# Kernel tuning notes

Hardware: AMD Instinct MI355X
Metric: run time of the kernel (lower is better)

## Reference

```python
import jax, jax.numpy as jnp
import numpy as np

D = 1024      # n_embd
NH = 16       # attention heads
E = 8         # n_experts
K = 2         # k_best
FF = 4 * D    # expert MLP hidden
EPS = 1e-6    # rms_norm_epsilon
TEMP = 1.0    # target_temperature


def setup_inputs() -> dict:
    key = jax.random.key(0)
    ks = jax.random.split(key, 12)
    B, S = 2, 1024
    s = 0.02
    return {
        "x": jax.random.normal(ks[0], (B, S, D), jnp.float32),
        "attn_norm_w": jnp.ones((D,), jnp.float32),
        "wq": jax.random.normal(ks[1], (D, D), jnp.float32) * s,
        "wk": jax.random.normal(ks[2], (D, D), jnp.float32) * s,
        "wv": jax.random.normal(ks[3], (D, D), jnp.float32) * s,
        "wo": jax.random.normal(ks[4], (D, D), jnp.float32) * s,
        "mlp_norm_w": jnp.ones((D,), jnp.float32),
        "router_w": jax.random.normal(ks[5], (D, E), jnp.float32) * s,
        "w1": jax.random.normal(ks[6], (E, D, FF), jnp.float32) * s,
        "b1": jnp.zeros((E, FF), jnp.float32),
        "w2": jax.random.normal(ks[7], (E, FF, D), jnp.float32) * s,
        "b2": jnp.zeros((E, D), jnp.float32),
    }


def _rmsnorm(x, w):
    var = jnp.mean(jnp.square(x), axis=-1, keepdims=True)
    return x * jax.lax.rsqrt(var + EPS) * w


def _attention(x, wq, wk, wv, wo):
    B, S, _ = x.shape
    dh = D // NH
    q = (x @ wq).reshape(B, S, NH, dh)
    k = (x @ wk).reshape(B, S, NH, dh)
    v = (x @ wv).reshape(B, S, NH, dh)
    scores = jnp.einsum("bqhd,bkhd->bhqk", q, k) / jnp.sqrt(jnp.float32(dh))
    causal = jnp.tril(jnp.ones((S, S), bool))  # [S,S]
    scores = jnp.where(causal[None, None], scores, jnp.finfo(scores.dtype).min)
    attn = jax.nn.softmax(scores, axis=-1)
    out = jnp.einsum("bhqk,bkhd->bqhd", attn, v).reshape(B, S, D)
    return out @ wo


def reference(x, attn_norm_w, wq, wk, wv, wo, mlp_norm_w, router_w, w1, b1, w2, b2):
    B, S, _ = x.shape
    # attention sub-block
    x = x + _attention(_rmsnorm(x, attn_norm_w), wq, wk, wv, wo)
    residual = x
    h = _rmsnorm(x, mlp_norm_w)  # [B,S,D]

    # router: temperature softmax + top-k
    logits = h @ router_w / TEMP                      # [B,S,E]
    probs = jax.nn.softmax(logits, axis=-1)
    top_k_scores, top_k_indices = jax.lax.top_k(probs, K)  # [B,S,K]
    onehot = jax.nn.one_hot(top_k_indices, E, dtype=h.dtype)  # [B,S,K,E]
    gates = jnp.einsum("bsk,bske->bse", top_k_scores, onehot)  # [B,S,E]

    # load-balancing loss (Switch-style) + expert counts
    counts = jnp.sum(onehot, axis=(0, 1, 2))          # [E]
    frac = counts / (B * S * K)
    mean_prob = jnp.mean(probs, axis=(0, 1))          # [E]
    balancing_loss = E * jnp.sum(frac * mean_prob)

    # experts: dense dispatch; tokens with zero gate contribute nothing,
    # so this matches the sort/gather/scatter top-k combine exactly.
    pre = jnp.einsum("bsd,edf->ebsf", h, w1) + b1[:, None, None]  # [E,B,S,FF]
    act = jax.nn.gelu(pre)
    y = jnp.einsum("ebsf,efd->ebsd", act, w2) + b2[:, None, None]  # [E,B,S,D]
    moe = jnp.einsum("ebsd,bse->bsd", y, gates)

    out = residual + moe
    return out, balancing_loss, counts
```

## Files before the change

### kernel.cpp

```cpp
#include <hip/hip_runtime.h>

typedef __bf16 bf16;
typedef __bf16 bf16x8 __attribute__((ext_vector_type(8)));
typedef float f32x4 __attribute__((ext_vector_type(4)));

#define D_   1024
#define S_   1024
#define B_   2
#define NTOK 2048
#define FF_  4096
#define NE   8
#define CAP  5120
#define OUTN 2097152

__device__ __forceinline__ float gelu_f(float x) {
    return 0.5f * x * (1.0f + tanhf(0.7978845608028654f * (x + 0.044715f * x * x * x)));
}

__global__ __launch_bounds__(256) void rmsnorm_k(const float* __restrict__ x,
                                                 const float* __restrict__ w,
                                                 float* __restrict__ yf,
                                                 bf16* __restrict__ yhi,
                                                 bf16* __restrict__ ylo) {
    int row = blockIdx.x;
    int t = threadIdx.x;
    const float* xr = x + (size_t)row * D_;
    float4 v = *(const float4*)(xr + t * 4);
    float ss = v.x * v.x + v.y * v.y + v.z * v.z + v.w * v.w;
    for (int off = 32; off; off >>= 1) ss += __shfl_down(ss, off);
    __shared__ float wsum[4];
    if ((t & 63) == 0) wsum[t >> 6] = ss;
    __syncthreads();
    float tot = wsum[0] + wsum[1] + wsum[2] + wsum[3];
    float rr = rsqrtf(tot * (1.0f / D_) + 1e-6f);
    float4 wv = *(const float4*)(w + t * 4);
    float y[4];
    y[0] = v.x * rr * wv.x; y[1] = v.y * rr * wv.y;
    y[2] = v.z * rr * wv.z; y[3] = v.w * rr * wv.w;
    if (yf) *(float4*)(yf + (size_t)row * D_ + t * 4) = *(float4*)y;
    if (yhi) {
#pragma unroll
        for (int i = 0; i < 4; i++) {
            bf16 hi = (bf16)y[i];
            yhi[(size_t)row * D_ + t * 4 + i] = hi;
            if (ylo) ylo[(size_t)row * D_ + t * 4 + i] = (bf16)(y[i] - (float)hi);
        }
    }
}

__global__ __launch_bounds__(256) void trans_split_k(
    const float* __restrict__ w0, const float* __restrict__ w1p,
    const float* __restrict__ w2p, const float* __restrict__ w3,
    bf16* o0h, bf16* o0l, bf16* o1h, bf16* o1l,
    bf16* o2h, bf16* o2l, bf16* o3h, bf16* o3l) {
    int z = blockIdx.z;
    const float* src = (z == 0) ? w0 : (z == 1) ? w1p : (z == 2) ? w2p : w3;
    bf16* dh = (z == 0) ? o0h : (z == 1) ? o1h : (z == 2) ? o2h : o3h;
    bf16* dl = (z == 0) ? o0l : (z == 1) ? o1l : (z == 2) ? o2l : o3l;
    __shared__ float tl[32][33];
    int c0 = blockIdx.x * 32, r0 = blockIdx.y * 32;
    int tx = threadIdx.x & 31, ty = threadIdx.x >> 5;
#pragma unroll
    for (int i = 0; i < 4; i++) {
        int r = ty + i * 8;
        tl[r][tx] = src[(size_t)(r0 + r) * 1024 + c0 + tx];
    }
    __syncthreads();
#pragma unroll
    for (int i = 0; i < 4; i++) {
        int c = ty + i * 8;
        float v = tl[tx][c];
        bf16 hi = (bf16)v;
        dh[(size_t)(c0 + c) * 1024 + r0 + tx] = hi;
        dl[(size_t)(c0 + c) * 1024 + r0 + tx] = (bf16)(v - (float)hi);
    }
}

__global__ __launch_bounds__(256) void transpose_cast_k(const float* __restrict__ in,
                                                        bf16* __restrict__ out,
                                                        int R, int C) {
    __shared__ float tl[32][33];
    size_t base = (size_t)blockIdx.z * R * C;
    const float* src = in + base;
    bf16* dst = out + base;
    int c0 = blockIdx.x * 32, r0 = blockIdx.y * 32;
    int tx = threadIdx.x & 31, tyy = threadIdx.x >> 5;
#pragma unroll
    for (int i = 0; i < 4; i++) {
        int r = tyy + i * 8;
        tl[r][tx] = src[(size_t)(r0 + r) * C + c0 + tx];
    }
    __syncthreads();
#pragma unroll
    for (int i = 0; i < 4; i++) {
        int c = tyy + i * 8;
        dst[(size_t)(c0 + c) * R + r0 + tx] = (bf16)tl[tx][c];
    }
}

#define GLD 40

#define GEMM_SPLIT_BODY(EPILOGUE)                                                     \
    __shared__ bf16 Ash[128 * GLD], Asl[128 * GLD], Bsh[128 * GLD], Bsl[128 * GLD];   \
    int t = threadIdx.x;                                                              \
    int m0 = blockIdx.x * 128, n0 = blockIdx.y * 128;                                 \
    int wv = t >> 6, ln = t & 63, wm = wv >> 1, wn = wv & 1;                          \
    int l15 = ln & 15, qd = ln >> 4;                                                  \
    f32x4 acc[4][4];                                                                  \
    _Pragma("unroll") for (int mt = 0; mt < 4; mt++)                                  \
        _Pragma("unroll") for (int nt = 0; nt < 4; nt++)                              \
            acc[mt][nt] = (f32x4){0.f, 0.f, 0.f, 0.f};                                \
    for (int k0 = 0; k0 < 1024; k0 += 32) {                                           \
        __syncthreads();                                                              \
        _Pragma("unroll") for (int j = 0; j < 2; j++) {                               \
            int idx = t + j * 256;                                                    \
            int row = idx >> 2, kc = (idx & 3) * 8;                                   \
            *(uint4*)&Ash[row * GLD + kc] = *(const uint4*)(Ah + (size_t)(m0 + row) * 1024 + k0 + kc); \
            *(uint4*)&Asl[row * GLD + kc] = *(const uint4*)(Al + (size_t)(m0 + row) * 1024 + k0 + kc); \
            *(uint4*)&Bsh[row * GLD + kc] = *(const uint4*)(Bh + (size_t)(n0 + row) * 1024 + k0 + kc); \
            *(uint4*)&Bsl[row * GLD + kc] = *(const uint4*)(Bl + (size_t)(n0 + row) * 1024 + k0 + kc); \
        }                                                                             \
        __syncthreads();                                                              \
        bf16x8 ah[4], al[4], bh[4], bl[4];                                            \
        _Pragma("unroll") for (int mt = 0; mt < 4; mt++) {                            \
            ah[mt] = *(const bf16x8*)&Ash[(wm * 64 + mt * 16 + l15) * GLD + qd * 8];  \
            al[mt] = *(const bf16x8*)&Asl[(wm * 64 + mt * 16 + l15) * GLD + qd * 8];  \
        }                                                                             \
        _Pragma("unroll") for (int nt = 0; nt < 4; nt++) {                            \
            bh[nt] = *(const bf16x8*)&Bsh[(wn * 64 + nt * 16 + l15) * GLD + qd * 8];  \
            bl[nt] = *(const bf16x8*)&Bsl[(wn * 64 + nt * 16 + l15) * GLD + qd * 8];  \
        }                                                                             \
        _Pragma("unroll") for (int mt = 0; mt < 4; mt++)                              \
            _Pragma("unroll") for (int nt = 0; nt < 4; nt++) {                        \
                acc[mt][nt] = __builtin_amdgcn_mfma_f32_16x16x32_bf16(ah[mt], bh[nt], acc[mt][nt], 0, 0, 0); \
                acc[mt][nt] = __builtin_amdgcn_mfma_f32_16x16x32_bf16(ah[mt], bl[nt], acc[mt][nt], 0, 0, 0); \
                acc[mt][nt] = __builtin_amdgcn_mfma_f32_16x16x32_bf16(al[mt], bh[nt], acc[mt][nt], 0, 0, 0); \
            }                                                                         \
    }                                                                                 \
    _Pragma("unroll") for (int mt = 0; mt < 4; mt++)                                  \
        _Pragma("unroll") for (int nt = 0; nt < 4; nt++) {                            \
            int gn = n0 + wn * 64 + nt * 16 + l15;                                    \
            _Pragma("unroll") for (int r = 0; r < 4; r++) {                           \
                int gm = m0 + wm * 64 + mt * 16 + qd * 4 + r;                         \
                float vv = acc[mt][nt][r];                                            \
                EPILOGUE                                                              \
            }                                                                         \
        }

__global__ __launch_bounds__(256) void gemm_split_qkv_k(
    const bf16* __restrict__ Ah, const bf16* __restrict__ Al,
    const bf16* __restrict__ Bqh, const bf16* __restrict__ Bql,
    const bf16* __restrict__ Bkh, const bf16* __restrict__ Bkl,
    const bf16* __restrict__ Bvh, const bf16* __restrict__ Bvl,
    bf16* Cqh, bf16* Cql, bf16* Ckh, bf16* Ckl, bf16* Cvh, bf16* Cvl) {
    int z = blockIdx.z;
    const bf16* Bh = (z == 0) ? Bqh : (z == 1) ? Bkh : Bvh;
    const bf16* Bl = (z == 0) ? Bql : (z == 1) ? Bkl : Bvl;
    bf16* Ch = (z == 0) ? Cqh : (z == 1) ? Ckh : Cvh;
    bf16* Cl = (z == 0) ? Cql : (z == 1) ? Ckl : Cvl;
    GEMM_SPLIT_BODY({
        bf16 hi = (bf16)vv;
        Ch[(size_t)gm * D_ + gn] = hi;
        Cl[(size_t)gm * D_ + gn] = (bf16)(vv - (float)hi);
    })
}

__global__ __launch_bounds__(256) void gemm_split_wo_k(
    const bf16* __restrict__ Ah, const bf16* __restrict__ Al,
    const bf16* __restrict__ Bh, const bf16* __restrict__ Bl,
    float* __restrict__ C, const float* __restrict__ X) {
    GEMM_SPLIT_BODY({
        C[(size_t)gm * D_ + gn] = X[(size_t)gm * D_ + gn] + vv;
    })
}

#define AP 72

__global__ __launch_bounds__(256) void attn_mfma_k(
    const bf16* __restrict__ qhp, const bf16* __restrict__ qlp,
    const bf16* __restrict__ khp, const bf16* __restrict__ klp,
    const bf16* __restrict__ vhp, const bf16* __restrict__ vlp,
    bf16* __restrict__ aoh, bf16* __restrict__ aol) {
    int qt = blockIdx.x, h = blockIdx.y, b = blockIdx.z;
    __shared__ bf16 Ksh[64 * AP], Ksl[64 * AP], VTh[64 * AP], VTl[64 * AP];
    __shared__ bf16 Ph[4][16 * AP], Pl[4][16 * AP];
    int t = threadIdx.x, wv = t >> 6, ln = t & 63, l15 = ln & 15, qd = ln >> 4;

    bf16x8 aqh[2], aql[2];
    {
        size_t qb = ((size_t)(b * S_ + qt * 64 + wv * 16 + l15)) * D_ + h * 64 + qd * 8;
        aqh[0] = *(const bf16x8*)(qhp + qb);
        aqh[1] = *(const bf16x8*)(qhp + qb + 32);
        aql[0] = *(const bf16x8*)(qlp + qb);
        aql[1] = *(const bf16x8*)(qlp + qb + 32);
    }
    f32x4 oacc[4];
    float mrow[4], lrow[4];
#pragma unroll
    for (int i = 0; i < 4; i++) {
        oacc[i] = (f32x4){0.f, 0.f, 0.f, 0.f};
        mrow[i] = -1e30f; lrow[i] = 0.0f;
    }

    for (int kt = 0; kt <= qt; kt++) {
        __syncthreads();
#pragma unroll
        for (int j = 0; j < 2; j++) {
            int idx = t + j * 256;
            int row = idx >> 3, ch = (idx & 7) * 8;
            size_t g = ((size_t)(b * S_ + kt * 64 + row)) * D_ + h * 64 + ch;
            *(uint4*)&Ksh[row * AP + ch] = *(const uint4*)(khp + g);
            *(uint4*)&Ksl[row * AP + ch] = *(const uint4*)(klp + g);
            bf16x8 vvh = *(const bf16x8*)(vhp + g);
            bf16x8 vvl = *(const bf16x8*)(vlp + g);
#pragma unroll
            for (int jj = 0; jj < 8; jj++) {
                VTh[(ch + jj) * AP + row] = vvh[jj];
                VTl[(ch + jj) * AP + row] = vvl[jj];
            }
        }
        __syncthreads();

        f32x4 sacc[4];
#pragma unroll
        for (int nt = 0; nt < 4; nt++) sacc[nt] = (f32x4){0.f, 0.f, 0.f, 0.f};
#pragma unroll
        for (int ks = 0; ks < 2; ks++) {
#pragma unroll
            for (int nt = 0; nt < 4; nt++) {
                bf16x8 bh = *(const bf16x8*)&Ksh[(nt * 16 + l15) * AP + ks * 32 + qd * 8];
                bf16x8 bl = *(const bf16x8*)&Ksl[(nt * 16 + l15) * AP + ks * 32 + qd * 8];
                sacc[nt] = __builtin_amdgcn_mfma_f32_16x16x32_bf16(aqh[ks], bh, sacc[nt], 0, 0, 0);
                sacc[nt] = __builtin_amdgcn_mfma_f32_16x16x32_bf16(aqh[ks], bl, sacc[nt], 0, 0, 0);
                sacc[nt] = __builtin_amdgcn_mfma_f32_16x16x32_bf16(aql[ks], bh, sacc[nt], 0, 0, 0);
            }
        }
        bool diag = (kt == qt);
#pragma unroll
        for (int r = 0; r < 4; r++) {
            float s0[4];
#pragma unroll
            for (int nt = 0; nt < 4; nt++) {
                s0[nt] = sacc[nt][r] * 0.125f;
                if (diag && (nt * 16 + l15) > (wv * 16 + qd * 4 + r)) s0[nt] = -1e30f;
            }
            float vmax = fmaxf(fmaxf(s0[0], s0[1]), fmaxf(s0[2], s0[3]));
            for (int off = 1; off < 16; off <<= 1) vmax = fmaxf(vmax, __shfl_xor(vmax, off));
            float mnew = fmaxf(mrow[r], vmax);
            float alpha = expf(mrow[r] - mnew);
            float p[4], rs = 0.0f;
#pragma unroll
            for (int nt = 0; nt < 4; nt++) { p[nt] = expf(s0[nt] - mnew); rs += p[nt]; }
            for (int off = 1; off < 16; off <<= 1) rs += __shfl_xor(rs, off);
            lrow[r] = lrow[r] * alpha + rs;
            mrow[r] = mnew;
#pragma unroll
            for (int nt = 0; nt < 4; nt++) oacc[nt][r] *= alpha;
            int prow = qd * 4 + r;
#pragma unroll
            for (int nt = 0; nt < 4; nt++) {
                bf16 hi = (bf16)p[nt];
                Ph[wv][prow * AP + nt * 16 + l15] = hi;
                Pl[wv][prow * AP + nt * 16 + l15] = (bf16)(p[nt] - (float)hi);
            }
        }
#pragma unroll
        for (int ks2 = 0; ks2 < 2; ks2++) {
            bf16x8 aph = *(const bf16x8*)&Ph[wv][l15 * AP + ks2 * 32 + qd * 8];
            bf16x8 apl = *(const bf16x8*)&Pl[wv][l15 * AP + ks2 * 32 + qd * 8];
#pragma unroll
            for (int nt = 0; nt < 4; nt++) {
                bf16x8 bvh = *(const bf16x8*)&VTh[(nt * 16 + l15) * AP + ks2 * 32 + qd * 8];
                bf16x8 bvl = *(const bf16x8*)&VTl[(nt * 16 + l15) * AP + ks2 * 32 + qd * 8];
                oacc[nt] = __builtin_amdgcn_mfma_f32_16x16x32_bf16(aph, bvh, oacc[nt], 0, 0, 0);
                oacc[nt] = __builtin_amdgcn_mfma_f32_16x16x32_bf16(aph, bvl, oacc[nt], 0, 0, 0);
                oacc[nt] = __builtin_amdgcn_mfma_f32_16x16x32_bf16(apl, bvh, oacc[nt], 0, 0, 0);
            }
        }
    }

#pragma unroll
    for (int r = 0; r < 4; r++) {
        float inv = 1.0f / lrow[r];
        size_t rowa = ((size_t)(b * S_ + qt * 64 + wv * 16 + qd * 4 + r)) * D_ + h * 64;
#pragma unroll
        for (int nt = 0; nt < 4; nt++) {
            float o = oacc[nt][r] * inv;
            bf16 hi = (bf16)o;
            aoh[rowa + nt * 16 + l15] = hi;
            aol[rowa + nt * 16 + l15] = (bf16)(o - (float)hi);
        }
    }
}

__global__ __launch_bounds__(256) void router_k(const float* __restrict__ h,
                                                const float* __restrict__ rw,
                                                int* __restrict__ tidx,
                                                float* __restrict__ tgate,
                                                int* __restrict__ ecnt,
                                                float* __restrict__ psum) {
    int wv = threadIdx.x >> 6, ln = threadIdx.x & 63;
    int tok = blockIdx.x * 4 + wv;
    const float* hr = h + (size_t)tok * D_;
    float acc[NE];
#pragma unroll
    for (int e = 0; e < NE; e++) acc[e] = 0.0f;
    int base = ln * 16;
#pragma unroll
    for (int c = 0; c < 4; c++) {
        float4 hv = *(const float4*)(hr + base + c * 4);
        const float* rp = rw + (size_t)(base + c * 4) * NE;
        float hx[4] = {hv.x, hv.y, hv.z, hv.w};
#pragma unroll
        for (int jj = 0; jj < 4; jj++)
#pragma unroll
            for (int e = 0; e < NE; e++)
                acc[e] = fmaf(hx[jj], rp[jj * NE + e], acc[e]);
    }
#pragma unroll
    for (int e = 0; e < NE; e++)
        for (int off = 32; off; off >>= 1) acc[e] += __shfl_down(acc[e], off);

    __shared__ float pb[4][NE];
    if (ln == 0) {
        float mx = acc[0];
#pragma unroll
        for (int e = 1; e < NE; e++) mx = fmaxf(mx, acc[e]);
        float p[NE], ssum = 0.0f;
#pragma unroll
        for (int e = 0; e < NE; e++) { p[e] = expf(acc[e] - mx); ssum += p[e]; }
        float inv = 1.0f / ssum;
#pragma unroll
        for (int e = 0; e < NE; e++) p[e] *= inv;
        int i0 = 0; float b0 = p[0];
#pragma unroll
        for (int e = 1; e < NE; e++) if (p[e] > b0) { b0 = p[e]; i0 = e; }
        int i1 = -1; float b1v = -1.0f;
#pragma unroll
        for (int e = 0; e < NE; e++) if (e != i0 && p[e] > b1v) { b1v = p[e]; i1 = e; }
        tidx[tok * 2] = i0; tidx[tok * 2 + 1] = i1;
        tgate[tok * 2] = b0; tgate[tok * 2 + 1] = b1v;
        atomicAdd(&ecnt[i0], 1);
        atomicAdd(&ecnt[i1], 1);
#pragma unroll
        for (int e = 0; e < NE; e++) pb[wv][e] = p[e];
    }
    __syncthreads();
    if (threadIdx.x < NE) {
        float s2 = pb[0][threadIdx.x] + pb[1][threadIdx.x] + pb[2][threadIdx.x] + pb[3][threadIdx.x];
        atomicAdd(&psum[threadIdx.x], s2);
    }
}

__global__ void passb_k(const int* __restrict__ ecnt, const float* __restrict__ psum,
                        int* __restrict__ eoffp, int* __restrict__ ecnt2,
                        float* __restrict__ out_tail) {
    if (threadIdx.x == 0) {
        int off = 0; float loss = 0.0f;
        for (int e = 0; e < NE; e++) {
            eoffp[e] = off;
            int c = ecnt[e];
            off += (c + 127) & ~127;
            loss += (c * (1.0f / 4096.0f)) * (psum[e] * (1.0f / 2048.0f));
            out_tail[1 + e] = (float)c;
            ecnt2[e] = 0;
        }
        eoffp[NE] = off;
        out_tail[0] = 8.0f * loss;
    }
}

__global__ __launch_bounds__(256) void scatter_k(const int* __restrict__ tidx,
                                                 const float* __restrict__ tgate,
                                                 const int* __restrict__ eoffp,
                                                 int* __restrict__ ecnt2,
                                                 int* __restrict__ stok,
                                                 float* __restrict__ sgate) {
    int tok = blockIdx.x * 256 + threadIdx.x;
    for (int k = 0; k < 2; k++) {
        int e = tidx[tok * 2 + k];
        int pos = eoffp[e] + atomicAdd(&ecnt2[e], 1);
        stok[pos] = tok;
        sgate[pos] = tgate[tok * 2 + k];
    }
}

#define MLD 40

__global__ __launch_bounds__(256) void moe_gemm1_k(const bf16* __restrict__ hB,
                                                   const bf16* __restrict__ w1t,
                                                   const float* __restrict__ b1,
                                                   const int* __restrict__ eoffp,
                                                   const int* __restrict__ stok,
                                                   bf16* __restrict__ act) {
    int m0 = blockIdx.x * 128, n0 = blockIdx.y * 128;
    if (m0 >= eoffp[NE]) return;
    int e = 0;
#pragma unroll
    for (int i = 1; i < NE; i++) if (m0 >= eoffp[i]) e = i;

    __shared__ bf16 As[128 * MLD];
    __shared__ bf16 Bs[128 * MLD];
    __shared__ int tok_l[128];
    int t = threadIdx.x;
    if (t < 128) tok_l[t] = stok[m0 + t];

    int wv = t >> 6, ln = t & 63;
    int wm = wv >> 1, wn = wv & 1;
    int lane15 = ln & 15, quad = ln >> 4;
    f32x4 acc[4][4];
#pragma unroll
    for (int mt = 0; mt < 4; mt++)
#pragma unroll
        for (int nt = 0; nt < 4; nt++) acc[mt][nt] = (f32x4){0.f, 0.f, 0.f, 0.f};

    const bf16* Bbase = w1t + ((size_t)e * FF_ + n0) * D_;

    for (int k0 = 0; k0 < D_; k0 += 32) {
        __syncthreads();
#pragma unroll
        for (int j = 0; j < 2; j++) {
            int idx = t + j * 256;
            int row = idx >> 2, kc = (idx & 3) * 8;
            uint4 av = *(const uint4*)(hB + (size_t)tok_l[row] * D_ + k0 + kc);
            *(uint4*)&As[row * MLD + kc] = av;
            uint4 bv = *(const uint4*)(Bbase + (size_t)row * D_ + k0 + kc);
            *(uint4*)&Bs[row * MLD + kc] = bv;
        }
        __syncthreads();
        bf16x8 af[4], bfr[4];
#pragma unroll
        for (int mt = 0; mt < 4; mt++)
            af[mt] = *(const bf16x8*)&As[(wm * 64 + mt * 16 + lane15) * MLD + quad * 8];
#pragma unroll
        for (int nt = 0; nt < 4; nt++)
            bfr[nt] = *(const bf16x8*)&Bs[(wn * 64 + nt * 16 + lane15) * MLD + quad * 8];
#pragma unroll
        for (int mt = 0; mt < 4; mt++)
#pragma unroll
            for (int nt = 0; nt < 4; nt++)
                acc[mt][nt] = __builtin_amdgcn_mfma_f32_16x16x32_bf16(af[mt], bfr[nt], acc[mt][nt], 0, 0, 0);
    }

    const float* b1e = b1 + (size_t)e * FF_;
#pragma unroll
    for (int mt = 0; mt < 4; mt++)
#pragma unroll
        for (int nt = 0; nt < 4; nt++) {
            int gn = n0 + wn * 64 + nt * 16 + lane15;
            float bias = b1e[gn];
#pragma unroll
            for (int r = 0; r < 4; r++) {
                int gm = m0 + wm * 64 + mt * 16 + quad * 4 + r;
                float vv = acc[mt][nt][r] + bias;
                act[(size_t)gm * FF_ + gn] = (bf16)gelu_f(vv);
            }
        }
}

__global__ __launch_bounds__(256) void moe_gemm2_k(const bf16* __restrict__ act,
                                                   const bf16* __restrict__ w2t,
                                                   const float* __restrict__ b2,
                                                   const int* __restrict__ eoffp,
                                                   const int* __restrict__ stok,
                                                   const float* __restrict__ sgate,
                                                   float* __restrict__ out) {
    int m0 = blockIdx.x * 128, n0 = blockIdx.y * 128;
    if (m0 >= eoffp[NE]) return;
    int e = 0;
#pragma unroll
    for (int i = 1; i < NE; i++) if (m0 >= eoffp[i]) e = i;

    __shared__ bf16 As[128 * MLD];
    __shared__ bf16 Bs[128 * MLD];
    __shared__ int tok_l[128];
    __shared__ float gate_l[128];
    int t = threadIdx.x;
    if (t < 128) { tok_l[t] = stok[m0 + t]; gate_l[t] = sgate[m0 + t]; }

    int wv = t >> 6, ln = t & 63;
    int wm = wv >> 1, wn = wv & 1;
    int lane15 = ln & 15, quad = ln >> 4;
    f32x4 acc[4][4];
#pragma unroll
    for (int mt = 0; mt < 4; mt++)
#pragma unroll
        for (int nt = 0; nt < 4; nt++) acc[mt][nt] = (f32x4){0.f, 0.f, 0.f, 0.f};

    const bf16* Bbase = w2t + ((size_t)e * D_ + n0) * FF_;

    for (int k0 = 0; k0 < FF_; k0 += 32) {
        __syncthreads();
#pragma unroll
        for (int j = 0; j < 2; j++) {
            int idx = t + j * 256;
            int row = idx >> 2, kc = (idx & 3) * 8;
            uint4 av = *(const uint4*)(act + (size_t)(m0 + row) * FF_ + k0 + kc);
            *(uint4*)&As[row * MLD + kc] = av;
            uint4 bv = *(const uint4*)(Bbase + (size_t)row * FF_ + k0 + kc);
            *(uint4*)&Bs[row * MLD + kc] = bv;
        }
        __syncthreads();
        bf16x8 af[4], bfr[4];
#pragma unroll
        for (int mt = 0; mt < 4; mt++)
            af[mt] = *(const bf16x8*)&As[(wm * 64 + mt * 16 + lane15) * MLD + quad * 8];
#pragma unroll
        for (int nt = 0; nt < 4; nt++)
            bfr[nt] = *(const bf16x8*)&Bs[(wn * 64 + nt * 16 + lane15) * MLD + quad * 8];
#pragma unroll
        for (int mt = 0; mt < 4; mt++)
#pragma unroll
            for (int nt = 0; nt < 4; nt++)
                acc[mt][nt] = __builtin_amdgcn_mfma_f32_16x16x32_bf16(af[mt], bfr[nt], acc[mt][nt], 0, 0, 0);
    }

    const float* b2e = b2 + (size_t)e * D_;
#pragma unroll
    for (int mt = 0; mt < 4; mt++)
#pragma unroll
        for (int nt = 0; nt < 4; nt++) {
            int gn = n0 + wn * 64 + nt * 16 + lane15;
            float bias = b2e[gn];
#pragma unroll
            for (int r = 0; r < 4; r++) {
                int lm = wm * 64 + mt * 16 + quad * 4 + r;
                int tok = tok_l[lm];
                float g = gate_l[lm];
                atomicAdd(out + (size_t)tok * D_ + gn, g * (acc[mt][nt][r] + bias));
            }
        }
}

extern "C" void kernel_launch(void* const* d_in, const int* in_sizes, int n_in,
                              void* d_out, int out_size, void* d_ws, size_t ws_size,
                              hipStream_t stream) {
    const float* x   = (const float*)d_in[0];
    const float* anw = (const float*)d_in[1];
    const float* wq  = (const float*)d_in[2];
    const float* wk  = (const float*)d_in[3];
    const float* wv  = (const float*)d_in[4];
    const float* wo  = (const float*)d_in[5];
    const float* mnw = (const float*)d_in[6];
    const float* rw  = (const float*)d_in[7];
    const float* w1  = (const float*)d_in[8];
    const float* b1  = (const float*)d_in[9];
    const float* w2  = (const float*)d_in[10];
    const float* b2  = (const float*)d_in[11];
    float* out = (float*)d_out;

    char* p = (char*)d_ws;
    auto take = [&](size_t n) { char* r = p; p += (n + 255) & ~(size_t)255; return r; };
    bf16* h1h = (bf16*)take((size_t)OUTN * 2);
    bf16* h1l = (bf16*)take((size_t)OUTN * 2);
    bf16* qh  = (bf16*)take((size_t)OUTN * 2);
    bf16* ql  = (bf16*)take((size_t)OUTN * 2);
    bf16* kh  = (bf16*)take((size_t)OUTN * 2);
    bf16* kl  = (bf16*)take((size_t)OUTN * 2);
    bf16* vh  = (bf16*)take((size_t)OUTN * 2);
    bf16* vl  = (bf16*)take((size_t)OUTN * 2);
    bf16* wqth = (bf16*)take((size_t)D_ * D_ * 2);
    bf16* wqtl = (bf16*)take((size_t)D_ * D_ * 2);
    bf16* wkth = (bf16*)take((size_t)D_ * D_ * 2);
    bf16* wktl = (bf16*)take((size_t)D_ * D_ * 2);
    bf16* wvth = (bf16*)take((size_t)D_ * D_ * 2);
    bf16* wvtl = (bf16*)take((size_t)D_ * D_ * 2);
    bf16* woth = (bf16*)take((size_t)D_ * D_ * 2);
    bf16* wotl = (bf16*)take((size_t)D_ * D_ * 2);
    bf16* w1t = (bf16*)take((size_t)NE * FF_ * D_ * 2);
    bf16* w2t = (bf16*)take((size_t)NE * FF_ * D_ * 2);
    bf16* act = (bf16*)take((size_t)CAP * FF_ * 2);
    int*   tidx  = (int*)take(NTOK * 2 * 4);
    float* tgate = (float*)take(NTOK * 2 * 4);
    int*   ecnt  = (int*)take(64);
    int*   ecnt2 = (int*)take(64);
    float* psum  = (float*)take(64);
    int*   eoffp = (int*)take(64);
    int*   stok  = (int*)take(CAP * 4);
    float* sgate = (float*)take(CAP * 4);

    bf16*  aoh = h1h;
    bf16*  aol = h1l;
    float* h_f = (float*)qh;
    bf16*  h_b = kh;

    hipMemsetAsync(ecnt, 0, NE * 4, stream);
    hipMemsetAsync(psum, 0, NE * 4, stream);
    hipMemsetAsync(stok, 0, CAP * 4, stream);
    hipMemsetAsync(sgate, 0, CAP * 4, stream);

    trans_split_k<<<dim3(32, 32, 4), 256, 0, stream>>>(wq, wk, wv, wo,
        wqth, wqtl, wkth, wktl, wvth, wvtl, woth, wotl);
    transpose_cast_k<<<dim3(FF_ / 32, D_ / 32, NE), 256, 0, stream>>>(w1, w1t, D_, FF_);
    transpose_cast_k<<<dim3(D_ / 32, FF_ / 32, NE), 256, 0, stream>>>(w2, w2t, FF_, D_);

    rmsnorm_k<<<NTOK, 256, 0, stream>>>(x, anw, nullptr, h1h, h1l);
    gemm_split_qkv_k<<<dim3(16, 8, 3), 256, 0, stream>>>(h1h, h1l,
        wqth, wqtl, wkth, wktl, wvth, wvtl,
        qh, ql, kh, kl, vh, vl);
    attn_mfma_k<<<dim3(16, 16, 2), 256, 0, stream>>>(qh, ql, kh, kl, vh, vl, aoh, aol);
    gemm_split_wo_k<<<dim3(16, 8), 256, 0, stream>>>(aoh, aol, woth, wotl, out, x);

    rmsnorm_k<<<NTOK, 256, 0, stream>>>(out, mnw, h_f, h_b, nullptr);
    router_k<<<NTOK / 4, 256, 0, stream>>>(h_f, rw, tidx, tgate, ecnt, psum);
    passb_k<<<1, 64, 0, stream>>>(ecnt, psum, eoffp, ecnt2, out + OUTN);
    scatter_k<<<NTOK / 256, 256, 0, stream>>>(tidx, tgate, eoffp, ecnt2, stok, sgate);
    moe_gemm1_k<<<dim3(CAP / 128, FF_ / 128), 256, 0, stream>>>(h_b, w1t, b1, eoffp, stok, act);
    moe_gemm2_k<<<dim3(CAP / 128, D_ / 128), 256, 0, stream>>>(act, w2t, b2, eoffp, stok, sgate, out);
}
```

Before: 900.1 us.

## Shrink GEMM tiles to 64x64, reverse attention tile order, replace atomic MoE combine

Switches the QKV, Wo and MoE second GEMMs from 128x128 to 64x64 tiles, giving four times as many workgroups on a device with many CUs. The attention grid now runs the heaviest causal query tiles first so the tail is better balanced. The MoE down-projection writes per-slot outputs to a buffer, and a separate combine kernel gathers each token's two expert rows with their gates, replacing scattered float atomics and making the result deterministic. In exchange, smaller tiles mean less operand reuse per block, and the combine adds an extra pass over the slot buffer.

```diff
diff --git a/kernel.cpp b/kernel.cpp
--- a/kernel.cpp
+++ b/kernel.cpp
@@ -100,77 +100,67 @@
 
 #define GLD 40
 
-#define GEMM_SPLIT_BODY(EPILOGUE)                                                     \
-    __shared__ bf16 Ash[128 * GLD], Asl[128 * GLD], Bsh[128 * GLD], Bsl[128 * GLD];   \
-    int t = threadIdx.x;                                                              \
-    int m0 = blockIdx.x * 128, n0 = blockIdx.y * 128;                                 \
-    int wv = t >> 6, ln = t & 63, wm = wv >> 1, wn = wv & 1;                          \
-    int l15 = ln & 15, qd = ln >> 4;                                                  \
-    f32x4 acc[4][4];                                                                  \
-    _Pragma("unroll") for (int mt = 0; mt < 4; mt++)                                  \
-        _Pragma("unroll") for (int nt = 0; nt < 4; nt++)                              \
-            acc[mt][nt] = (f32x4){0.f, 0.f, 0.f, 0.f};                                \
-    for (int k0 = 0; k0 < 1024; k0 += 32) {                                           \
-        __syncthreads();                                                              \
-        _Pragma("unroll") for (int j = 0; j < 2; j++) {                               \
-            int idx = t + j * 256;                                                    \
-            int row = idx >> 2, kc = (idx & 3) * 8;                                   \
-            *(uint4*)&Ash[row * GLD + kc] = *(const uint4*)(Ah + (size_t)(m0 + row) * 1024 + k0 + kc); \
-            *(uint4*)&Asl[row * GLD + kc] = *(const uint4*)(Al + (size_t)(m0 + row) * 1024 + k0 + kc); \
-            *(uint4*)&Bsh[row * GLD + kc] = *(const uint4*)(Bh + (size_t)(n0 + row) * 1024 + k0 + kc); \
-            *(uint4*)&Bsl[row * GLD + kc] = *(const uint4*)(Bl + (size_t)(n0 + row) * 1024 + k0 + kc); \
-        }                                                                             \
-        __syncthreads();                                                              \
-        bf16x8 ah[4], al[4], bh[4], bl[4];                                            \
-        _Pragma("unroll") for (int mt = 0; mt < 4; mt++) {                            \
-            ah[mt] = *(const bf16x8*)&Ash[(wm * 64 + mt * 16 + l15) * GLD + qd * 8];  \
-            al[mt] = *(const bf16x8*)&Asl[(wm * 64 + mt * 16 + l15) * GLD + qd * 8];  \
-        }                                                                             \
-        _Pragma("unroll") for (int nt = 0; nt < 4; nt++) {                            \
-            bh[nt] = *(const bf16x8*)&Bsh[(wn * 64 + nt * 16 + l15) * GLD + qd * 8];  \
-            bl[nt] = *(const bf16x8*)&Bsl[(wn * 64 + nt * 16 + l15) * GLD + qd * 8];  \
-        }                                                                             \
-        _Pragma("unroll") for (int mt = 0; mt < 4; mt++)                              \
-            _Pragma("unroll") for (int nt = 0; nt < 4; nt++) {                        \
-                acc[mt][nt] = __builtin_amdgcn_mfma_f32_16x16x32_bf16(ah[mt], bh[nt], acc[mt][nt], 0, 0, 0); \
-                acc[mt][nt] = __builtin_amdgcn_mfma_f32_16x16x32_bf16(ah[mt], bl[nt], acc[mt][nt], 0, 0, 0); \
-                acc[mt][nt] = __builtin_amdgcn_mfma_f32_16x16x32_bf16(al[mt], bh[nt], acc[mt][nt], 0, 0, 0); \
-            }                                                                         \
-    }                                                                                 \
-    _Pragma("unroll") for (int mt = 0; mt < 4; mt++)                                  \
-        _Pragma("unroll") for (int nt = 0; nt < 4; nt++) {                            \
-            int gn = n0 + wn * 64 + nt * 16 + l15;                                    \
-            _Pragma("unroll") for (int r = 0; r < 4; r++) {                           \
-                int gm = m0 + wm * 64 + mt * 16 + qd * 4 + r;                         \
-                float vv = acc[mt][nt][r];                                            \
-                EPILOGUE                                                              \
-            }                                                                         \
-        }
-
-__global__ __launch_bounds__(256) void gemm_split_qkv_k(
+#define GEMM64_SPLIT_BODY(N0EXPR, EPILOGUE)                                            \
+    __shared__ bf16 Ash[64 * GLD], Asl[64 * GLD], Bsh[64 * GLD], Bsl[64 * GLD];        \
+    int t = threadIdx.x;                                                               \
+    int m0 = blockIdx.x * 64;                                                          \
+    int n0 = (N0EXPR);                                                                 \
+    int wv = t >> 6, ln = t & 63, l15 = ln & 15, qd = ln >> 4;                         \
+    int srow = t >> 2, skc = (t & 3) * 8;                                              \
+    f32x4 acc[4];                                                                      \
+    _Pragma("unroll") for (int mt = 0; mt < 4; mt++) acc[mt] = (f32x4){0.f,0.f,0.f,0.f}; \
+    for (int k0 = 0; k0 < 1024; k0 += 32) {                                            \
+        __syncthreads();                                                               \
+        *(bf16x8*)&Ash[srow * GLD + skc] = *(const bf16x8*)(Ah + (size_t)(m0 + srow) * 1024 + k0 + skc); \
+        *(bf16x8*)&Asl[srow * GLD + skc] = *(const bf16x8*)(Al + (size_t)(m0 + srow) * 1024 + k0 + skc); \
+        *(bf16x8*)&Bsh[srow * GLD + skc] = *(const bf16x8*)(Bh + (size_t)(n0 + srow) * 1024 + k0 + skc); \
+        *(bf16x8*)&Bsl[srow * GLD + skc] = *(const bf16x8*)(Bl + (size_t)(n0 + srow) * 1024 + k0 + skc); \
+        __syncthreads();                                                               \
+        bf16x8 ah[4], al[4];                                                           \
+        _Pragma("unroll") for (int mt = 0; mt < 4; mt++) {                             \
+            ah[mt] = *(const bf16x8*)&Ash[(mt * 16 + l15) * GLD + qd * 8];             \
+            al[mt] = *(const bf16x8*)&Asl[(mt * 16 + l15) * GLD + qd * 8];             \
+        }                                                                              \
+        bf16x8 bh = *(const bf16x8*)&Bsh[(wv * 16 + l15) * GLD + qd * 8];              \
+        bf16x8 bl = *(const bf16x8*)&Bsl[(wv * 16 + l15) * GLD + qd * 8];              \
+        _Pragma("unroll") for (int mt = 0; mt < 4; mt++) {                             \
+            acc[mt] = __builtin_amdgcn_mfma_f32_16x16x32_bf16(ah[mt], bh, acc[mt], 0, 0, 0); \
+            acc[mt] = __builtin_amdgcn_mfma_f32_16x16x32_bf16(ah[mt], bl, acc[mt], 0, 0, 0); \
+            acc[mt] = __builtin_amdgcn_mfma_f32_16x16x32_bf16(al[mt], bh, acc[mt], 0, 0, 0); \
+        }                                                                              \
+    }                                                                                  \
+    int gnl = wv * 16 + l15;                                                           \
+    _Pragma("unroll") for (int mt = 0; mt < 4; mt++)                                   \
+        _Pragma("unroll") for (int r = 0; r < 4; r++) {                                \
+            int gm = m0 + mt * 16 + qd * 4 + r;                                        \
+            float vv = acc[mt][r];                                                     \
+            EPILOGUE                                                                   \
+        }
+
+__global__ __launch_bounds__(256) void gemm_qkv_k(
     const bf16* __restrict__ Ah, const bf16* __restrict__ Al,
     const bf16* __restrict__ Bqh, const bf16* __restrict__ Bql,
     const bf16* __restrict__ Bkh, const bf16* __restrict__ Bkl,
     const bf16* __restrict__ Bvh, const bf16* __restrict__ Bvl,
     bf16* Cqh, bf16* Cql, bf16* Ckh, bf16* Ckl, bf16* Cvh, bf16* Cvl) {
-    int z = blockIdx.z;
-    const bf16* Bh = (z == 0) ? Bqh : (z == 1) ? Bkh : Bvh;
-    const bf16* Bl = (z == 0) ? Bql : (z == 1) ? Bkl : Bvl;
-    bf16* Ch = (z == 0) ? Cqh : (z == 1) ? Ckh : Cvh;
-    bf16* Cl = (z == 0) ? Cql : (z == 1) ? Ckl : Cvl;
-    GEMM_SPLIT_BODY({
+    int gy = blockIdx.y, zw = gy >> 4;
+    const bf16* Bh = (zw == 0) ? Bqh : (zw == 1) ? Bkh : Bvh;
+    const bf16* Bl = (zw == 0) ? Bql : (zw == 1) ? Bkl : Bvl;
+    bf16* Ch = (zw == 0) ? Cqh : (zw == 1) ? Ckh : Cvh;
+    bf16* Cl = (zw == 0) ? Cql : (zw == 1) ? Ckl : Cvl;
+    GEMM64_SPLIT_BODY((gy & 15) * 64, {
         bf16 hi = (bf16)vv;
-        Ch[(size_t)gm * D_ + gn] = hi;
-        Cl[(size_t)gm * D_ + gn] = (bf16)(vv - (float)hi);
+        Ch[(size_t)gm * D_ + n0 + gnl] = hi;
+        Cl[(size_t)gm * D_ + n0 + gnl] = (bf16)(vv - (float)hi);
     })
 }
 
-__global__ __launch_bounds__(256) void gemm_split_wo_k(
+__global__ __launch_bounds__(256) void gemm_wo_k(
     const bf16* __restrict__ Ah, const bf16* __restrict__ Al,
     const bf16* __restrict__ Bh, const bf16* __restrict__ Bl,
     float* __restrict__ C, const float* __restrict__ X) {
-    GEMM_SPLIT_BODY({
-        C[(size_t)gm * D_ + gn] = X[(size_t)gm * D_ + gn] + vv;
+    GEMM64_SPLIT_BODY(blockIdx.y * 64, {
+        C[(size_t)gm * D_ + n0 + gnl] = X[(size_t)gm * D_ + n0 + gnl] + vv;
     })
 }
 
@@ -181,7 +171,8 @@
     const bf16* __restrict__ khp, const bf16* __restrict__ klp,
     const bf16* __restrict__ vhp, const bf16* __restrict__ vlp,
     bf16* __restrict__ aoh, bf16* __restrict__ aol) {
-    int qt = blockIdx.x, h = blockIdx.y, b = blockIdx.z;
+    int qt = (int)gridDim.x - 1 - (int)blockIdx.x;
+    int h = blockIdx.y, b = blockIdx.z;
     __shared__ bf16 Ksh[64 * AP], Ksl[64 * AP], VTh[64 * AP], VTl[64 * AP];
     __shared__ bf16 Ph[4][16 * AP], Pl[4][16 * AP];
     int t = threadIdx.x, wv = t >> 6, ln = t & 63, l15 = ln & 15, qd = ln >> 4;
@@ -209,8 +200,8 @@
             int idx = t + j * 256;
             int row = idx >> 3, ch = (idx & 7) * 8;
             size_t g = ((size_t)(b * S_ + kt * 64 + row)) * D_ + h * 64 + ch;
-            *(uint4*)&Ksh[row * AP + ch] = *(const uint4*)(khp + g);
-            *(uint4*)&Ksl[row * AP + ch] = *(const uint4*)(klp + g);
+            *(bf16x8*)&Ksh[row * AP + ch] = *(const bf16x8*)(khp + g);
+            *(bf16x8*)&Ksl[row * AP + ch] = *(const bf16x8*)(klp + g);
             bf16x8 vvh = *(const bf16x8*)(vhp + g);
             bf16x8 vvl = *(const bf16x8*)(vlp + g);
 #pragma unroll
@@ -371,17 +362,16 @@
 }
 
 __global__ __launch_bounds__(256) void scatter_k(const int* __restrict__ tidx,
-                                                 const float* __restrict__ tgate,
                                                  const int* __restrict__ eoffp,
                                                  int* __restrict__ ecnt2,
                                                  int* __restrict__ stok,
-                                                 float* __restrict__ sgate) {
+                                                 int* __restrict__ sidx) {
     int tok = blockIdx.x * 256 + threadIdx.x;
     for (int k = 0; k < 2; k++) {
         int e = tidx[tok * 2 + k];
         int pos = eoffp[e] + atomicAdd(&ecnt2[e], 1);
         stok[pos] = tok;
-        sgate[pos] = tgate[tok * 2 + k];
+        sidx[tok * 2 + k] = pos;
     }
 }
 
@@ -462,74 +452,68 @@
                                                    const bf16* __restrict__ w2t,
                                                    const float* __restrict__ b2,
                                                    const int* __restrict__ eoffp,
-                                                   const int* __restrict__ stok,
-                                                   const float* __restrict__ sgate,
-                                                   float* __restrict__ out) {
-    int m0 = blockIdx.x * 128, n0 = blockIdx.y * 128;
+                                                   float* __restrict__ y) {
+    int m0 = blockIdx.x * 64;
     if (m0 >= eoffp[NE]) return;
     int e = 0;
 #pragma unroll
     for (int i = 1; i < NE; i++) if (m0 >= eoffp[i]) e = i;
-
-    __shared__ bf16 As[128 * MLD];
-    __shared__ bf16 Bs[128 * MLD];
-    __shared__ int tok_l[128];
-    __shared__ float gate_l[128];
+    int n0 = blockIdx.y * 64;
+
+    __shared__ bf16 As[64 * MLD];
+    __shared__ bf16 Bs[64 * MLD];
     int t = threadIdx.x;
-    if (t < 128) { tok_l[t] = stok[m0 + t]; gate_l[t] = sgate[m0 + t]; }
-
-    int wv = t >> 6, ln = t & 63;
-    int wm = wv >> 1, wn = wv & 1;
-    int lane15 = ln & 15, quad = ln >> 4;
-    f32x4 acc[4][4];
-#pragma unroll
-    for (int mt = 0; mt < 4; mt++)
-#pragma unroll
-        for (int nt = 0; nt < 4; nt++) acc[mt][nt] = (f32x4){0.f, 0.f, 0.f, 0.f};
+    int wv = t >> 6, ln = t & 63, l15 = ln & 15, qd = ln >> 4;
+    int srow = t >> 2, skc = (t & 3) * 8;
+
+    f32x4 acc[4];
+#pragma unroll
+    for (int mt = 0; mt < 4; mt++) acc[mt] = (f32x4){0.f, 0.f, 0.f, 0.f};
 
     const bf16* Bbase = w2t + ((size_t)e * D_ + n0) * FF_;
 
     for (int k0 = 0; k0 < FF_; k0 += 32) {
         __syncthreads();
-#pragma unroll
-        for (int j = 0; j < 2; j++) {
-            int idx = t + j * 256;
-            int row = idx >> 2, kc = (idx & 3) * 8;
-            uint4 av = *(const uint4*)(act + (size_t)(m0 + row) * FF_ + k0 + kc);
-            *(uint4*)&As[row * MLD + kc] = av;
-            uint4 bv = *(const uint4*)(Bbase + (size_t)row * FF_ + k0 + kc);
-            *(uint4*)&Bs[row * MLD + kc] = bv;
-        }
+        *(bf16x8*)&As[srow * MLD + skc] = *(const bf16x8*)(act + (size_t)(m0 + srow) * FF_ + k0 + skc);
+        *(bf16x8*)&Bs[srow * MLD + skc] = *(const bf16x8*)(Bbase + (size_t)srow * FF_ + k0 + skc);
         __syncthreads();
-        bf16x8 af[4], bfr[4];
+        bf16x8 af[4];
 #pragma unroll
         for (int mt = 0; mt < 4; mt++)
-            af[mt] = *(const bf16x8*)&As[(wm * 64 + mt * 16 + lane15) * MLD + quad * 8];
-#pragma unroll
-        for (int nt = 0; nt < 4; nt++)
-            bfr[nt] = *(const bf16x8*)&Bs[(wn * 64 + nt * 16 + lane15) * MLD + quad * 8];
+            af[mt] = *(const bf16x8*)&As[(mt * 16 + l15) * MLD + qd * 8];
+        bf16x8 bfr = *(const bf16x8*)&Bs[(wv * 16 + l15) * MLD + qd * 8];
 #pragma unroll
         for (int mt = 0; mt < 4; mt++)
-#pragma unroll
-            for (int nt = 0; nt < 4; nt++)
-                acc[mt][nt] = __builtin_amdgcn_mfma_f32_16x16x32_bf16(af[mt], bfr[nt], acc[mt][nt], 0, 0, 0);
-    }
-
-    const float* b2e = b2 + (size_t)e * D_;
+            acc[mt] = __builtin_amdgcn_mfma_f32_16x16x32_bf16(af[mt], bfr, acc[mt], 0, 0, 0);
+    }
+
+    int gn = n0 + wv * 16 + l15;
+    float bias = b2[(size_t)e * D_ + gn];
 #pragma unroll
     for (int mt = 0; mt < 4; mt++)
 #pragma unroll
-        for (int nt = 0; nt < 4; nt++) {
-            int gn = n0 + wn * 64 + nt * 16 + lane15;
-            float bias = b2e[gn];
-#pragma unroll
-            for (int r = 0; r < 4; r++) {
-                int lm = wm * 64 + mt * 16 + quad * 4 + r;
-                int tok = tok_l[lm];
-                float g = gate_l[lm];
-                atomicAdd(out + (size_t)tok * D_ + gn, g * (acc[mt][nt][r] + bias));
-            }
-        }
+        for (int r = 0; r < 4; r++) {
+            int gm = m0 + mt * 16 + qd * 4 + r;
+            y[(size_t)gm * D_ + gn] = acc[mt][r] + bias;
+        }
+}
+
+__global__ __launch_bounds__(256) void combine_k(const float* __restrict__ y,
+                                                 const int* __restrict__ sidx,
+                                                 const float* __restrict__ tgate,
+                                                 float* __restrict__ out) {
+    int tok = blockIdx.x;
+    int d = threadIdx.x * 4;
+    int s0 = sidx[tok * 2], s1 = sidx[tok * 2 + 1];
+    float g0 = tgate[tok * 2], g1 = tgate[tok * 2 + 1];
+    float4 a = *(const float4*)(y + (size_t)s0 * D_ + d);
+    float4 b = *(const float4*)(y + (size_t)s1 * D_ + d);
+    float4 o = *(const float4*)(out + (size_t)tok * D_ + d);
+    o.x += g0 * a.x + g1 * b.x;
+    o.y += g0 * a.y + g1 * b.y;
+    o.z += g0 * a.z + g1 * b.z;
+    o.w += g0 * a.w + g1 * b.w;
+    *(float4*)(out + (size_t)tok * D_ + d) = o;
 }
 
 extern "C" void kernel_launch(void* const* d_in, const int* in_sizes, int n_in,
@@ -572,22 +556,22 @@
     bf16* act = (bf16*)take((size_t)CAP * FF_ * 2);
     int*   tidx  = (int*)take(NTOK * 2 * 4);
     float* tgate = (float*)take(NTOK * 2 * 4);
+    int*   sidx  = (int*)take(NTOK * 2 * 4);
     int*   ecnt  = (int*)take(64);
     int*   ecnt2 = (int*)take(64);
     float* psum  = (float*)take(64);
     int*   eoffp = (int*)take(64);
     int*   stok  = (int*)take(CAP * 4);
-    float* sgate = (float*)take(CAP * 4);
 
     bf16*  aoh = h1h;
     bf16*  aol = h1l;
     float* h_f = (float*)qh;
     bf16*  h_b = kh;
+    float* y   = (float*)vh;
 
     hipMemsetAsync(ecnt, 0, NE * 4, stream);
     hipMemsetAsync(psum, 0, NE * 4, stream);
     hipMemsetAsync(stok, 0, CAP * 4, stream);
-    hipMemsetAsync(sgate, 0, CAP * 4, stream);
 
     trans_split_k<<<dim3(32, 32, 4), 256, 0, stream>>>(wq, wk, wv, wo,
         wqth, wqtl, wkth, wktl, wvth, wvtl, woth, wotl);
@@ -595,16 +579,16 @@
     transpose_cast_k<<<dim3(D_ / 32, FF_ / 32, NE), 256, 0, stream>>>(w2, w2t, FF_, D_);
 
     rmsnorm_k<<<NTOK, 256, 0, stream>>>(x, anw, nullptr, h1h, h1l);
-    gemm_split_qkv_k<<<dim3(16, 8, 3), 256, 0, stream>>>(h1h, h1l,
-        wqth, wqtl, wkth, wktl, wvth, wvtl,
-        qh, ql, kh, kl, vh, vl);
+    gemm_qkv_k<<<dim3(32, 48), 256, 0, stream>>>(h1h, h1l,
+        wqth, wqtl, wkth, wktl, wvth, wvtl, qh, ql, kh, kl, vh, vl);
     attn_mfma_k<<<dim3(16, 16, 2), 256, 0, stream>>>(qh, ql, kh, kl, vh, vl, aoh, aol);
-    gemm_split_wo_k<<<dim3(16, 8), 256, 0, stream>>>(aoh, aol, woth, wotl, out, x);
+    gemm_wo_k<<<dim3(32, 16), 256, 0, stream>>>(aoh, aol, woth, wotl, out, x);
 
     rmsnorm_k<<<NTOK, 256, 0, stream>>>(out, mnw, h_f, h_b, nullptr);
     router_k<<<NTOK / 4, 256, 0, stream>>>(h_f, rw, tidx, tgate, ecnt, psum);
     passb_k<<<1, 64, 0, stream>>>(ecnt, psum, eoffp, ecnt2, out + OUTN);
-    scatter_k<<<NTOK / 256, 256, 0, stream>>>(tidx, tgate, eoffp, ecnt2, stok, sgate);
+    scatter_k<<<NTOK / 256, 256, 0, stream>>>(tidx, eoffp, ecnt2, stok, sidx);
     moe_gemm1_k<<<dim3(CAP / 128, FF_ / 128), 256, 0, stream>>>(h_b, w1t, b1, eoffp, stok, act);
-    moe_gemm2_k<<<dim3(CAP / 128, D_ / 128), 256, 0, stream>>>(act, w2t, b2, eoffp, stok, sgate, out);
-}
+    moe_gemm2_k<<<dim3(CAP / 64, D_ / 64), 256, 0, stream>>>(act, w2t, b2, eoffp, y);
+    combine_k<<<NTOK, 256, 0, stream>>>(y, sidx, tgate, out);
+}
```

Result: faster. 842.1 us (-6.4%).
